# Optimization experiments

Measured on AMD Instinct MI355X. Metric: run time of the kernel, lower is better.

The kernel has to match this reference:

```python
import jax, jax.numpy as jnp
import numpy as np

D_MODEL = 2048
N_HEAD = 32
N_KV_HEAD = 8
N_REP = N_HEAD // N_KV_HEAD
D_K = D_MODEL // N_HEAD
THETA = 10000.0
B, S = 2, 1024


def setup_inputs() -> dict:
    key = jax.random.key(0)
    ks = jax.random.split(key, 9)
    sd = 1.0 / np.sqrt(D_MODEL)
    return {
        "x": jax.random.normal(ks[0], (B, S, D_MODEL), jnp.float32),
        "Wq": jax.random.normal(ks[1], (D_MODEL, D_MODEL), jnp.float32) * sd,
        "bq": jax.random.normal(ks[2], (D_MODEL,), jnp.float32) * 0.02,
        "Wk": jax.random.normal(ks[3], (D_MODEL, N_KV_HEAD * D_K), jnp.float32) * sd,
        "bk": jax.random.normal(ks[4], (N_KV_HEAD * D_K,), jnp.float32) * 0.02,
        "Wv": jax.random.normal(ks[5], (D_MODEL, N_KV_HEAD * D_K), jnp.float32) * sd,
        "bv": jax.random.normal(ks[6], (N_KV_HEAD * D_K,), jnp.float32) * 0.02,
        "Wo": jax.random.normal(ks[7], (D_MODEL, D_MODEL), jnp.float32) * sd,
        "bo": jax.random.normal(ks[8], (D_MODEL,), jnp.float32) * 0.02,
    }


def _apply_rope(t, pos):
    # t: [b, h, s, d_k], pos: [s]
    half = D_K // 2
    inv_freq = 1.0 / (THETA ** (jnp.arange(half, dtype=jnp.float32) * 2.0 / D_K))
    ang = pos[:, None].astype(jnp.float32) * inv_freq[None, :]  # [s, half]
    cos = jnp.cos(ang)[None, None]  # [1,1,s,half]
    sin = jnp.sin(ang)[None, None]
    te = t[..., 0::2]
    to = t[..., 1::2]
    re = te * cos - to * sin
    ro = te * sin + to * cos
    return jnp.stack([re, ro], axis=-1).reshape(t.shape)


def reference(x, Wq, bq, Wk, bk, Wv, bv, Wo, bo):
    b, s, _ = x.shape
    q = (x @ Wq + bq).reshape(b, s, N_HEAD, D_K).transpose(0, 2, 1, 3)
    k = (x @ Wk + bk).reshape(b, s, N_KV_HEAD, D_K).transpose(0, 2, 1, 3)
    v = (x @ Wv + bv).reshape(b, s, N_KV_HEAD, D_K).transpose(0, 2, 1, 3)
    pos = jnp.arange(s)
    q = _apply_rope(q, pos)
    k = _apply_rope(k, pos)
    # GQA head repeat: [b, n_kv, s, d] -> [b, n_head, s, d]
    k = jnp.repeat(k, N_REP, axis=1)
    v = jnp.repeat(v, N_REP, axis=1)
    scores = jnp.einsum('bhnd,bhmd->bhnm', q, k) / jnp.sqrt(jnp.float32(D_K))
    mask = jnp.tril(jnp.ones((s, s), dtype=bool))
    scores = jnp.where(mask[None, None], scores, jnp.float32(-jnp.inf))
    probs = jax.nn.softmax(scores, axis=-1)
    out = jnp.einsum('bhnm,bhmd->bhnd', probs, v)
    out = out.transpose(0, 2, 1, 3).reshape(b, s, D_MODEL)
    return out @ Wo + bo
```

## Files before the change

### kernel.cpp

```cpp
#include <hip/hip_runtime.h>
#include <hip/hip_bf16.h>

#define D_MODEL 2048
#define N_HEAD 32
#define N_KV_HEAD 8
#define N_REP 4
#define D_K 64
#define S_LEN 1024
#define B_SZ 2
#define M_ROWS (B_SZ * S_LEN)
#define KV_DIM (N_KV_HEAD * D_K)
#define QKV_N 3072
#define KOFF 2048
#define VOFF 2560
#define LOG2E 1.44269504088896f

typedef __attribute__((ext_vector_type(8))) short short8;
typedef __attribute__((ext_vector_type(4))) float f32x4;

#define EXP2F(x) __builtin_amdgcn_exp2f(x)

__device__ inline unsigned short f2bf(float f) {
    union { float f; unsigned int u; } x{f};
    unsigned int r = x.u + 0x7fffu + ((x.u >> 16) & 1u);
    return (unsigned short)(r >> 16);
}
__device__ inline float bf2f(unsigned short b) {
    union { unsigned int u; float f; } x; x.u = ((unsigned int)b) << 16; return x.f;
}
__device__ inline void store_c(float* p, float v) { *p = v; }
__device__ inline void store_c(unsigned short* p, float v) { *p = f2bf(v); }

__device__ inline void load_lds16(const unsigned short* g, unsigned short* l) {
    __builtin_amdgcn_global_load_lds(
        (const __attribute__((address_space(1))) unsigned int*)g,
        (__attribute__((address_space(3))) unsigned int*)l, 16, 0, 0);
}

__global__ void transpose_cast_kernel(const float* __restrict__ W,
                                      unsigned short* __restrict__ Wt,
                                      int K, int N) {
    __shared__ float tile[32][33];
    int n0 = blockIdx.x * 32, k0 = blockIdx.y * 32;
    int tx = threadIdx.x, ty = threadIdx.y;
#pragma unroll
    for (int r = 0; r < 4; r++)
        tile[ty * 4 + r][tx] = W[(size_t)(k0 + ty * 4 + r) * N + n0 + tx];
    __syncthreads();
#pragma unroll
    for (int r = 0; r < 4; r++)
        Wt[(size_t)(n0 + ty * 4 + r) * K + k0 + tx] = f2bf(tile[tx][ty * 4 + r]);
}

__global__ void cast_bf_kernel(const float* __restrict__ src,
                               unsigned short* __restrict__ dst, int n4) {
    int idx = blockIdx.x * blockDim.x + threadIdx.x;
    if (idx >= n4) return;
    float4 v = ((const float4*)src)[idx];
    unsigned int lo = (unsigned int)f2bf(v.x) | ((unsigned int)f2bf(v.y) << 16);
    unsigned int hi = (unsigned int)f2bf(v.z) | ((unsigned int)f2bf(v.w) << 16);
    ((uint2*)dst)[idx] = make_uint2(lo, hi);
}

__global__ void concat_bias_kernel(const float* __restrict__ bq, const float* __restrict__ bk,
                                   const float* __restrict__ bv, float* __restrict__ dst) {
    int i = blockIdx.x * blockDim.x + threadIdx.x;
    if (i >= QKV_N) return;
    dst[i] = (i < KOFF) ? bq[i] : (i < VOFF) ? bk[i - KOFF] : bv[i - VOFF];
}

template <typename TC>
__global__ __launch_bounds__(256) void gemm_bf16_kernel(
        const unsigned short* __restrict__ A,
        const unsigned short* __restrict__ Bt,
        const float* __restrict__ bias,
        TC* __restrict__ C, int M, int N, int K) {
    __shared__ unsigned short As[128 * 64];
    __shared__ unsigned short Bs[64 * 64];
    const int tid = threadIdx.x, lane = tid & 63;
    const int w = tid >> 6, wm = w >> 1, wn = w & 1;
    const int quad = lane >> 4, lr = lane & 15;
    const int bm = blockIdx.y * 128, bn = blockIdx.x * 64;

    f32x4 acc[4][2];
#pragma unroll
    for (int i = 0; i < 4; i++)
#pragma unroll
        for (int j = 0; j < 2; j++) acc[i][j] = (f32x4){0.f, 0.f, 0.f, 0.f};

    for (int k0 = 0; k0 < K; k0 += 64) {
        __syncthreads();
#pragma unroll
        for (int it = 0; it < 4; it++) {
            int slot = it * 256 + tid;
            int row = slot >> 3;
            int qc = (slot & 7) ^ (row & 7);
            load_lds16(A + (size_t)(bm + row) * K + k0 + qc * 8, &As[slot * 8]);
        }
#pragma unroll
        for (int it = 0; it < 2; it++) {
            int slot = it * 256 + tid;
            int row = slot >> 3;
            int qc = (slot & 7) ^ (row & 7);
            load_lds16(Bt + (size_t)(bn + row) * K + k0 + qc * 8, &Bs[slot * 8]);
        }
        __syncthreads();
#pragma unroll
        for (int ks = 0; ks < 2; ks++) {
            short8 af[4], bf[2];
#pragma unroll
            for (int i = 0; i < 4; i++) {
                int row = wm * 64 + i * 16 + lr;
                af[i] = *(const short8*)&As[(row * 8 + ((ks * 4 + quad) ^ (lr & 7))) * 8];
            }
#pragma unroll
            for (int j = 0; j < 2; j++) {
                int row = wn * 32 + j * 16 + lr;
                bf[j] = *(const short8*)&Bs[(row * 8 + ((ks * 4 + quad) ^ (lr & 7))) * 8];
            }
#pragma unroll
            for (int i = 0; i < 4; i++)
#pragma unroll
                for (int j = 0; j < 2; j++)
                    acc[i][j] = __builtin_amdgcn_mfma_f32_16x16x32_bf16(af[i], bf[j], acc[i][j], 0, 0, 0);
        }
    }
#pragma unroll
    for (int i = 0; i < 4; i++) {
#pragma unroll
        for (int j = 0; j < 2; j++) {
            int col = bn + wn * 32 + j * 16 + lr;
            int row0 = bm + wm * 64 + i * 16 + quad * 4;
            float bj = bias[col];
#pragma unroll
            for (int r = 0; r < 4; r++)
                store_c(&C[(size_t)(row0 + r) * N + col], acc[i][j][r] + bj);
        }
    }
}

__global__ void rope_bf_kernel(unsigned short* __restrict__ t) {
    const int QI = M_ROWS * N_HEAD * 32;
    const int TOT = QI + M_ROWS * N_KV_HEAD * 32;
    int idx = blockIdx.x * blockDim.x + threadIdx.x;
    if (idx >= TOT) return;
    int col_off, n_heads;
    float scale;
    if (idx < QI) { col_off = 0; n_heads = N_HEAD; scale = 0.125f * LOG2E; }
    else { idx -= QI; col_off = KOFF; n_heads = N_KV_HEAD; scale = 1.0f; }
    int i = idx & 31;
    int hh = (idx >> 5) % n_heads;
    int r = idx / (32 * n_heads);
    int s = r % S_LEN;
    float inv_freq = powf(10000.0f, -2.0f * (float)i / 64.0f);
    float ang = (float)s * inv_freq;
    float c = cosf(ang), sn = sinf(ang);
    unsigned short* p = t + (size_t)r * QKV_N + col_off + hh * D_K + 2 * i;
    float te = bf2f(p[0]), to = bf2f(p[1]);
    p[0] = f2bf((te * c - to * sn) * scale);
    p[1] = f2bf((te * sn + to * c) * scale);
}

#define AST 72
__device__ __forceinline__ void attn_tile(
        int w, int quad, int lr, bool diag,
        const unsigned short* Ks, const unsigned short* Vt, unsigned short* Ps,
        const short8* aq, f32x4* oacc, float* mrow, float* lrow) {
    f32x4 s[4];
#pragma unroll
    for (int cf = 0; cf < 4; cf++) s[cf] = (f32x4){0.f, 0.f, 0.f, 0.f};
#pragma unroll
    for (int ks = 0; ks < 2; ks++) {
#pragma unroll
        for (int cf = 0; cf < 4; cf++) {
            short8 bk = *(const short8*)&Ks[(cf * 16 + lr) * AST + ks * 32 + quad * 8];
            s[cf] = __builtin_amdgcn_mfma_f32_16x16x32_bf16(aq[ks], bk, s[cf], 0, 0, 0);
        }
    }
    if (diag) {
#pragma unroll
        for (int cf = 0; cf < 4; cf++) {
            int key = cf * 16 + lr;
#pragma unroll
            for (int r = 0; r < 4; r++)
                if (key > w * 16 + quad * 4 + r) s[cf][r] = -1e30f;
        }
    }
    float corr[4];
#pragma unroll
    for (int r = 0; r < 4; r++) {
        float rm = fmaxf(fmaxf(s[0][r], s[1][r]), fmaxf(s[2][r], s[3][r]));
        rm = fmaxf(rm, __shfl_xor(rm, 1));
        rm = fmaxf(rm, __shfl_xor(rm, 2));
        rm = fmaxf(rm, __shfl_xor(rm, 4));
        rm = fmaxf(rm, __shfl_xor(rm, 8));
        float mn = fmaxf(mrow[r], rm);
        corr[r] = EXP2F(mrow[r] - mn);
        mrow[r] = mn;
        float rs = 0.f;
#pragma unroll
        for (int cf = 0; cf < 4; cf++) {
            float p = EXP2F(s[cf][r] - mn);
            union { float f; unsigned int u; } px{p};
            px.u &= 0xFFFF0000u;
            Ps[(w * 16 + quad * 4 + r) * AST + cf * 16 + lr] =
                (unsigned short)(px.u >> 16);
            rs += px.f;
        }
        rs += __shfl_xor(rs, 1);
        rs += __shfl_xor(rs, 2);
        rs += __shfl_xor(rs, 4);
        rs += __shfl_xor(rs, 8);
        lrow[r] = lrow[r] * corr[r] + rs;
    }
#pragma unroll
    for (int cf = 0; cf < 4; cf++)
#pragma unroll
        for (int r = 0; r < 4; r++) oacc[cf][r] *= corr[r];
#pragma unroll
    for (int ks = 0; ks < 2; ks++) {
        short8 ap = *(const short8*)&Ps[(w * 16 + lr) * AST + ks * 32 + quad * 8];
#pragma unroll
        for (int cf = 0; cf < 4; cf++) {
            short8 bv = *(const short8*)&Vt[(cf * 16 + lr) * AST + ks * 32 + quad * 8];
            oacc[cf] = __builtin_amdgcn_mfma_f32_16x16x32_bf16(ap, bv, oacc[cf], 0, 0, 0);
        }
    }
}

__global__ __launch_bounds__(256) void attn_mfma_kernel(
        const unsigned short* __restrict__ qkv,
        unsigned short* __restrict__ obf) {
    __shared__ unsigned short Ks[64 * AST];
    __shared__ unsigned short Vt[64 * AST];
    __shared__ unsigned short Ps[64 * AST];
    const int tid = threadIdx.x;
    const int w = tid >> 6, lane = tid & 63;
    const int lr = lane & 15, quad = lane >> 4;
    const int h = blockIdx.y, b = blockIdx.z;
    const int kvh = h >> 2;
    const unsigned short* kb = qkv + (size_t)(b * S_LEN) * QKV_N + KOFF + kvh * D_K;
    const unsigned short* vb = qkv + (size_t)(b * S_LEN) * QKV_N + VOFF + kvh * D_K;

    const int qtA = blockIdx.x;
    const int qtB = 15 - qtA;
    const int ntA = qtA + 1, ntB = qtB + 1;

    short8 aqA[2], aqB[2];
    {
        const unsigned short* qp = qkv + (size_t)(b * S_LEN + qtA * 64 + w * 16 + lr) * QKV_N
                                   + h * D_K + quad * 8;
        aqA[0] = *(const short8*)qp;
        aqA[1] = *(const short8*)(qp + 32);
        qp = qkv + (size_t)(b * S_LEN + qtB * 64 + w * 16 + lr) * QKV_N + h * D_K + quad * 8;
        aqB[0] = *(const short8*)qp;
        aqB[1] = *(const short8*)(qp + 32);
    }
    f32x4 oaccA[4], oaccB[4];
#pragma unroll
    for (int cf = 0; cf < 4; cf++) {
        oaccA[cf] = (f32x4){0.f, 0.f, 0.f, 0.f};
        oaccB[cf] = (f32x4){0.f, 0.f, 0.f, 0.f};
    }
    float mA[4] = {-1e30f, -1e30f, -1e30f, -1e30f}, lA[4] = {0.f, 0.f, 0.f, 0.f};
    float mB[4] = {-1e30f, -1e30f, -1e30f, -1e30f}, lB[4] = {0.f, 0.f, 0.f, 0.f};

    for (int t = 0; t < ntB; t++) {
        const int j0 = t * 64;
        __syncthreads();
#pragma unroll
        for (int it = 0; it < 2; it++) {
            int f = it * 256 + tid;
            int key = f >> 3, d8 = (f & 7) * 8;
            *(uint4*)&Ks[key * AST + d8] =
                *(const uint4*)(kb + (size_t)(j0 + key) * QKV_N + d8);
        }
        {
            int kp = tid & 31, dg = tid >> 5;
            unsigned short ta[8], tb[8];
            *(uint4*)ta = *(const uint4*)(vb + (size_t)(j0 + 2 * kp) * QKV_N + dg * 8);
            *(uint4*)tb = *(const uint4*)(vb + (size_t)(j0 + 2 * kp + 1) * QKV_N + dg * 8);
#pragma unroll
            for (int i = 0; i < 8; i++) {
                unsigned int pk = (unsigned int)ta[i] | ((unsigned int)tb[i] << 16);
                *(unsigned int*)&Vt[(dg * 8 + i) * AST + 2 * kp] = pk;
            }
        }
        __syncthreads();
        if (t < ntA)
            attn_tile(w, quad, lr, t == qtA, Ks, Vt, Ps, aqA, oaccA, mA, lA);
        attn_tile(w, quad, lr, t == qtB, Ks, Vt, Ps, aqB, oaccB, mB, lB);
    }
#pragma unroll
    for (int r = 0; r < 4; r++) {
        float invA = 1.f / lA[r], invB = 1.f / lB[r];
        int rowA = b * S_LEN + qtA * 64 + w * 16 + quad * 4 + r;
        int rowB = b * S_LEN + qtB * 64 + w * 16 + quad * 4 + r;
#pragma unroll
        for (int cf = 0; cf < 4; cf++) {
            obf[(size_t)rowA * D_MODEL + h * D_K + cf * 16 + lr] = f2bf(oaccA[cf][r] * invA);
            obf[(size_t)rowB * D_MODEL + h * D_K + cf * 16 + lr] = f2bf(oaccB[cf][r] * invB);
        }
    }
}

extern "C" void kernel_launch(void* const* d_in, const int* in_sizes, int n_in,
                              void* d_out, int out_size, void* d_ws, size_t ws_size,
                              hipStream_t stream) {
    const float* x  = (const float*)d_in[0];
    const float* Wq = (const float*)d_in[1];
    const float* bq = (const float*)d_in[2];
    const float* Wk = (const float*)d_in[3];
    const float* bk = (const float*)d_in[4];
    const float* Wv = (const float*)d_in[5];
    const float* bv = (const float*)d_in[6];
    const float* Wo = (const float*)d_in[7];
    const float* bo = (const float*)d_in[8];
    float* out = (float*)d_out;

    unsigned short* xbf   = (unsigned short*)d_ws;
    unsigned short* WtQKV = xbf + (size_t)M_ROWS * D_MODEL;
    unsigned short* WtO   = WtQKV + (size_t)QKV_N * D_MODEL;
    unsigned short* qkv   = WtO + (size_t)D_MODEL * D_MODEL;
    float* bias_qkv       = (float*)(qkv + (size_t)M_ROWS * QKV_N);
    unsigned short* obf   = xbf;

    dim3 tb(32, 8);
    dim3 gb(256);

    cast_bf_kernel<<<(M_ROWS * D_MODEL / 4 + 255) / 256, gb, 0, stream>>>(x, xbf, M_ROWS * D_MODEL / 4);
    transpose_cast_kernel<<<dim3(D_MODEL / 32, D_MODEL / 32), tb, 0, stream>>>(Wq, WtQKV, D_MODEL, D_MODEL);
    transpose_cast_kernel<<<dim3(KV_DIM / 32, D_MODEL / 32), tb, 0, stream>>>(Wk, WtQKV + (size_t)KOFF * D_MODEL, D_MODEL, KV_DIM);
    transpose_cast_kernel<<<dim3(KV_DIM / 32, D_MODEL / 32), tb, 0, stream>>>(Wv, WtQKV + (size_t)VOFF * D_MODEL, D_MODEL, KV_DIM);
    transpose_cast_kernel<<<dim3(D_MODEL / 32, D_MODEL / 32), tb, 0, stream>>>(Wo, WtO, D_MODEL, D_MODEL);
    concat_bias_kernel<<<(QKV_N + 255) / 256, gb, 0, stream>>>(bq, bk, bv, bias_qkv);
    gemm_bf16_kernel<unsigned short><<<dim3(QKV_N / 64, M_ROWS / 128), gb, 0, stream>>>(
        xbf, WtQKV, bias_qkv, qkv, M_ROWS, QKV_N, D_MODEL);
    rope_bf_kernel<<<(M_ROWS * (N_HEAD + N_KV_HEAD) * 32 + 255) / 256, gb, 0, stream>>>(qkv);
    attn_mfma_kernel<<<dim3(8, N_HEAD, B_SZ), gb, 0, stream>>>(qkv, obf);
    gemm_bf16_kernel<float><<<dim3(D_MODEL / 64, M_ROWS / 128), gb, 0, stream>>>(
        obf, WtO, bo, out, M_ROWS, D_MODEL, D_MODEL);
}
```

Measured before the change: 242.4 us.

## Merge weight transposes, use fast RoPE intrinsics, one query tile per attention block

Folds the four weight transpose-casts into one launch with a direct global-read, packed-store scheme and no LDS tile. RoPE now computes inverse frequencies with exp2 and uses the fast __sinf/__cosf intrinsics instead of powf/sinf/cosf. The attention kernel no longer pairs two causal query tiles per block. It launches 16 blocks per head, each handling one tile with the heaviest tiles scheduled first, which doubles parallelism but loses the K/V reuse between paired tiles. The fast sin/cos may lose some accuracy at large angles.

```diff
diff --git a/kernel.cpp b/kernel.cpp
--- a/kernel.cpp
+++ b/kernel.cpp
@@ -37,19 +37,33 @@
         (__attribute__((address_space(3))) unsigned int*)l, 16, 0, 0);
 }
 
-__global__ void transpose_cast_kernel(const float* __restrict__ W,
-                                      unsigned short* __restrict__ Wt,
-                                      int K, int N) {
-    __shared__ float tile[32][33];
-    int n0 = blockIdx.x * 32, k0 = blockIdx.y * 32;
-    int tx = threadIdx.x, ty = threadIdx.y;
-#pragma unroll
-    for (int r = 0; r < 4; r++)
-        tile[ty * 4 + r][tx] = W[(size_t)(k0 + ty * 4 + r) * N + n0 + tx];
-    __syncthreads();
-#pragma unroll
-    for (int r = 0; r < 4; r++)
-        Wt[(size_t)(n0 + ty * 4 + r) * K + k0 + tx] = f2bf(tile[tx][ty * 4 + r]);
+__global__ __launch_bounds__(256) void wprep_kernel(
+        const float* __restrict__ Wq_, const float* __restrict__ Wk_,
+        const float* __restrict__ Wv_, const float* __restrict__ Wo_,
+        unsigned short* __restrict__ WtQKV, unsigned short* __restrict__ WtO) {
+    const float* src; unsigned short* dst; int N;
+    switch (blockIdx.z) {
+        case 0: src = Wq_; dst = WtQKV; N = D_MODEL; break;
+        case 1: src = Wk_; dst = WtQKV + (size_t)KOFF * D_MODEL; N = KV_DIM; break;
+        case 2: src = Wv_; dst = WtQKV + (size_t)VOFF * D_MODEL; N = KV_DIM; break;
+        default: src = Wo_; dst = WtO; N = D_MODEL; break;
+    }
+    int n0 = blockIdx.x * 64;
+    if (n0 >= N) return;
+    int k0 = blockIdx.y * 64;
+    int t = threadIdx.x;
+    int n = n0 + (t >> 2);
+    int ks = k0 + (t & 3) * 16;
+    unsigned int pk[8];
+#pragma unroll
+    for (int i = 0; i < 8; i++) {
+        float a = src[(size_t)(ks + 2 * i) * N + n];
+        float b = src[(size_t)(ks + 2 * i + 1) * N + n];
+        pk[i] = (unsigned int)f2bf(a) | ((unsigned int)f2bf(b) << 16);
+    }
+    uint4* d = (uint4*)&dst[(size_t)n * D_MODEL + ks];
+    d[0] = make_uint4(pk[0], pk[1], pk[2], pk[3]);
+    d[1] = make_uint4(pk[4], pk[5], pk[6], pk[7]);
 }
 
 __global__ void cast_bf_kernel(const float* __restrict__ src,
@@ -152,9 +166,9 @@
     int hh = (idx >> 5) % n_heads;
     int r = idx / (32 * n_heads);
     int s = r % S_LEN;
-    float inv_freq = powf(10000.0f, -2.0f * (float)i / 64.0f);
+    float inv_freq = EXP2F((float)i * -0.41524101186f);
     float ang = (float)s * inv_freq;
-    float c = cosf(ang), sn = sinf(ang);
+    float c = __cosf(ang), sn = __sinf(ang);
     unsigned short* p = t + (size_t)r * QKV_N + col_off + hh * D_K + 2 * i;
     float te = bf2f(p[0]), to = bf2f(p[1]);
     p[0] = f2bf((te * c - to * sn) * scale);
@@ -242,30 +256,23 @@
     const unsigned short* kb = qkv + (size_t)(b * S_LEN) * QKV_N + KOFF + kvh * D_K;
     const unsigned short* vb = qkv + (size_t)(b * S_LEN) * QKV_N + VOFF + kvh * D_K;
 
-    const int qtA = blockIdx.x;
-    const int qtB = 15 - qtA;
-    const int ntA = qtA + 1, ntB = qtB + 1;
-
-    short8 aqA[2], aqB[2];
+    const int qt = 15 - (int)blockIdx.x;
+    const int q0 = qt * 64;
+
+    short8 aq[2];
     {
-        const unsigned short* qp = qkv + (size_t)(b * S_LEN + qtA * 64 + w * 16 + lr) * QKV_N
+        const unsigned short* qp = qkv + (size_t)(b * S_LEN + q0 + w * 16 + lr) * QKV_N
                                    + h * D_K + quad * 8;
-        aqA[0] = *(const short8*)qp;
-        aqA[1] = *(const short8*)(qp + 32);
-        qp = qkv + (size_t)(b * S_LEN + qtB * 64 + w * 16 + lr) * QKV_N + h * D_K + quad * 8;
-        aqB[0] = *(const short8*)qp;
-        aqB[1] = *(const short8*)(qp + 32);
-    }
-    f32x4 oaccA[4], oaccB[4];
-#pragma unroll
-    for (int cf = 0; cf < 4; cf++) {
-        oaccA[cf] = (f32x4){0.f, 0.f, 0.f, 0.f};
-        oaccB[cf] = (f32x4){0.f, 0.f, 0.f, 0.f};
-    }
-    float mA[4] = {-1e30f, -1e30f, -1e30f, -1e30f}, lA[4] = {0.f, 0.f, 0.f, 0.f};
-    float mB[4] = {-1e30f, -1e30f, -1e30f, -1e30f}, lB[4] = {0.f, 0.f, 0.f, 0.f};
-
-    for (int t = 0; t < ntB; t++) {
+        aq[0] = *(const short8*)qp;
+        aq[1] = *(const short8*)(qp + 32);
+    }
+    f32x4 oacc[4];
+#pragma unroll
+    for (int cf = 0; cf < 4; cf++) oacc[cf] = (f32x4){0.f, 0.f, 0.f, 0.f};
+    float mrow[4] = {-1e30f, -1e30f, -1e30f, -1e30f};
+    float lrow[4] = {0.f, 0.f, 0.f, 0.f};
+
+    for (int t = 0; t <= qt; t++) {
         const int j0 = t * 64;
         __syncthreads();
 #pragma unroll
@@ -287,20 +294,15 @@
             }
         }
         __syncthreads();
-        if (t < ntA)
-            attn_tile(w, quad, lr, t == qtA, Ks, Vt, Ps, aqA, oaccA, mA, lA);
-        attn_tile(w, quad, lr, t == qtB, Ks, Vt, Ps, aqB, oaccB, mB, lB);
+        attn_tile(w, quad, lr, t == qt, Ks, Vt, Ps, aq, oacc, mrow, lrow);
     }
 #pragma unroll
     for (int r = 0; r < 4; r++) {
-        float invA = 1.f / lA[r], invB = 1.f / lB[r];
-        int rowA = b * S_LEN + qtA * 64 + w * 16 + quad * 4 + r;
-        int rowB = b * S_LEN + qtB * 64 + w * 16 + quad * 4 + r;
-#pragma unroll
-        for (int cf = 0; cf < 4; cf++) {
-            obf[(size_t)rowA * D_MODEL + h * D_K + cf * 16 + lr] = f2bf(oaccA[cf][r] * invA);
-            obf[(size_t)rowB * D_MODEL + h * D_K + cf * 16 + lr] = f2bf(oaccB[cf][r] * invB);
-        }
+        float inv = 1.f / lrow[r];
+        int row = b * S_LEN + q0 + w * 16 + quad * 4 + r;
+#pragma unroll
+        for (int cf = 0; cf < 4; cf++)
+            obf[(size_t)row * D_MODEL + h * D_K + cf * 16 + lr] = f2bf(oacc[cf][r] * inv);
     }
 }
 
@@ -325,19 +327,15 @@
     float* bias_qkv       = (float*)(qkv + (size_t)M_ROWS * QKV_N);
     unsigned short* obf   = xbf;
 
-    dim3 tb(32, 8);
     dim3 gb(256);
 
     cast_bf_kernel<<<(M_ROWS * D_MODEL / 4 + 255) / 256, gb, 0, stream>>>(x, xbf, M_ROWS * D_MODEL / 4);
-    transpose_cast_kernel<<<dim3(D_MODEL / 32, D_MODEL / 32), tb, 0, stream>>>(Wq, WtQKV, D_MODEL, D_MODEL);
-    transpose_cast_kernel<<<dim3(KV_DIM / 32, D_MODEL / 32), tb, 0, stream>>>(Wk, WtQKV + (size_t)KOFF * D_MODEL, D_MODEL, KV_DIM);
-    transpose_cast_kernel<<<dim3(KV_DIM / 32, D_MODEL / 32), tb, 0, stream>>>(Wv, WtQKV + (size_t)VOFF * D_MODEL, D_MODEL, KV_DIM);
-    transpose_cast_kernel<<<dim3(D_MODEL / 32, D_MODEL / 32), tb, 0, stream>>>(Wo, WtO, D_MODEL, D_MODEL);
+    wprep_kernel<<<dim3(32, 32, 4), gb, 0, stream>>>(Wq, Wk, Wv, Wo, WtQKV, WtO);
     concat_bias_kernel<<<(QKV_N + 255) / 256, gb, 0, stream>>>(bq, bk, bv, bias_qkv);
     gemm_bf16_kernel<unsigned short><<<dim3(QKV_N / 64, M_ROWS / 128), gb, 0, stream>>>(
         xbf, WtQKV, bias_qkv, qkv, M_ROWS, QKV_N, D_MODEL);
     rope_bf_kernel<<<(M_ROWS * (N_HEAD + N_KV_HEAD) * 32 + 255) / 256, gb, 0, stream>>>(qkv);
-    attn_mfma_kernel<<<dim3(8, N_HEAD, B_SZ), gb, 0, stream>>>(qkv, obf);
+    attn_mfma_kernel<<<dim3(16, N_HEAD, B_SZ), gb, 0, stream>>>(qkv, obf);
     gemm_bf16_kernel<float><<<dim3(D_MODEL / 64, M_ROWS / 128), gb, 0, stream>>>(
         obf, WtO, bo, out, M_ROWS, D_MODEL, D_MODEL);
 }
```

After: 249.2 us. 1.03x slower.
